# Kernel optimization log

Hardware: AMD Instinct MI355X
Metric: run time of the kernel (lower is better)

Reference implementation:

```python
import jax, jax.numpy as jnp
import numpy as np
import math

PS = 65          # patch_size
NB_ANG = 8       # num_ang_bins
NB_SP = 4        # num_spatial_bins
CLIP = 0.2
EPS = 1e-10
BIN_KS = 2 * (PS // (NB_SP + 1))   # 26
BIN_STRIDE = PS // NB_SP           # 16
BIN_PAD = BIN_KS // 4              # 6


def _gaussian_kernel2d(ks, sigma):
    x = jnp.arange(ks, dtype=jnp.float32) - ks // 2
    if ks % 2 == 0:
        x = x + 0.5
    g = jnp.exp(-(x * x) / (2.0 * sigma * sigma))
    g = g / g.sum()
    return jnp.outer(g, g)  # [ps, ps]


def _sift_pooling_kernel(ks):
    ks2 = ks / 2.0
    xc2 = ks2 - jnp.abs(jnp.arange(ks, dtype=jnp.float32) + 0.5 - ks2)
    return jnp.outer(xc2, xc2) / (ks2 * ks2)  # [26, 26] triangular bilinear kernel


def _l2n(x):
    # torch F.normalize(p=2, dim=-1, eps=1e-12)
    return x / jnp.maximum(jnp.linalg.norm(x, axis=-1, keepdims=True), 1e-12)


def setup_inputs() -> dict:
    key = jax.random.key(0)
    image_batch = jax.random.uniform(key, (16, 3, 520, 520), dtype=jnp.float32)
    return {"image_batch": image_batch}


def reference(image_batch):
    B, C, H, W = image_batch.shape
    nH, nW = H // PS, W // PS
    # torch unfold(2,ps,ps).unfold(3,ps,ps).reshape(-1, c, ps, ps)
    # (row-major reshape replicated exactly, including its channel/patch mixing)
    p = image_batch.reshape(B, C, nH, PS, nW, PS).transpose(0, 1, 2, 4, 3, 5)
    x = p.reshape(-1, C, PS, PS)  # [N, C, ps, ps]; (N,C) treated as independent patches
    N = x.shape[0]

    # kornia spatial_gradient(mode='diff', normalized=True): replicate pad, central diff / 2
    xp = jnp.pad(x, ((0, 0), (0, 0), (1, 1), (1, 1)), mode='edge')
    gx = (xp[:, :, 1:-1, 2:] - xp[:, :, 1:-1, :-2]) * 0.5
    gy = (xp[:, :, 2:, 1:-1] - xp[:, :, :-2, 1:-1]) * 0.5

    mag = jnp.sqrt(gx * gx + gy * gy + EPS)
    ori = jnp.arctan2(gy, gx + EPS) + 2.0 * jnp.pi
    gk = _gaussian_kernel2d(PS, PS / math.sqrt(2.0))
    mag = mag * gk  # Gaussian spatial weighting

    # soft orientation binning
    o_big = (NB_ANG / (2.0 * jnp.pi)) * ori
    bo0f = jnp.floor(o_big)
    wo1 = o_big - bo0f
    bo0 = (bo0f % NB_ANG).astype(jnp.int32)
    bo1 = (bo0 + 1) % NB_ANG
    # [N, C, ps, ps, 8] soft histogram field
    contrib = (jax.nn.one_hot(bo0, NB_ANG, dtype=x.dtype) * ((1.0 - wo1) * mag)[..., None]
               + jax.nn.one_hot(bo1, NB_ANG, dtype=x.dtype) * (wo1 * mag)[..., None])

    # spatial pooling: conv 26x26, stride 16, zero-pad 6 -> 4x4 per angle bin
    contrib = jnp.moveaxis(contrib, -1, 2).reshape(N * C * NB_ANG, 1, PS, PS)
    pk = _sift_pooling_kernel(BIN_KS)[None, None]  # [1,1,26,26]
    pooled = jax.lax.conv_general_dilated(
        contrib, pk,
        window_strides=(BIN_STRIDE, BIN_STRIDE),
        padding=((BIN_PAD, BIN_PAD), (BIN_PAD, BIN_PAD)),
        dimension_numbers=('NCHW', 'OIHW', 'NCHW'))  # [N*C*8, 1, 4, 4]

    desc = pooled.reshape(N, C, NB_ANG * NB_SP * NB_SP)  # [N, C, 128]
    desc = _l2n(desc)
    desc = jnp.clip(desc, 0.0, CLIP)
    desc = _l2n(desc)
    return desc  # [B*nH*nW, C, 128] (root_sift=False)
```

## Files before the change

kernel.cpp:

```cpp
#include <hip/hip_runtime.h>
#include <math.h>

#define PSTR 33

constexpr double cfabs_(double x) { return x < 0 ? -x : x; }
constexpr double cexp_neg(double x) {
    double t = 1.0, s = 1.0;
    for (int i = 1; i < 20; ++i) { t *= (-x) / i; s += t; }
    return s;
}
constexpr double graw(int i) {
    double d = (double)(i - 32);
    return cexp_neg(d * d / 4225.0);
}
constexpr double gsum_() { double s = 0; for (int i = 0; i < 65; ++i) s += graw(i); return s; }
constexpr double GSUM_V = gsum_();
constexpr float gnv(int i) { return (float)(graw(i) / GSUM_V); }

struct WTab { float a[65]; };
constexpr WTab mkw(int sy) {
    WTab w{};
    for (int i = 0; i < 65; ++i) {
        double t = 13.0 - cfabs_((double)i - 16.0 * sy - 6.5);
        w.a[i] = (float)((graw(i) / GSUM_V) * t / 13.0);
    }
    return w;
}
constexpr WTab WGTBL[4] = { mkw(0), mkw(1), mkw(2), mkw(3) };
#define WGTG(SY, RR) (WGTBL[SY].a[RR])
constexpr float G64F = gnv(64);

#define G4_(n) gnv(n), gnv(n+1), gnv(n+2), gnv(n+3)
__device__ __constant__ float d_gtab[65] = {
    G4_(0), G4_(4), G4_(8), G4_(12), G4_(16), G4_(20), G4_(24), G4_(28),
    G4_(32), G4_(36), G4_(40), G4_(44), G4_(48), G4_(52), G4_(56), G4_(60),
    gnv(64)
};

__device__ __forceinline__ float fast_atan2f(float y, float x) {
    float ax = fabsf(x), ay = fabsf(y);
    float mx = fmaxf(ax, ay);
    float mn = fminf(ax, ay);
    float a = mn * __builtin_amdgcn_rcpf(fmaxf(mx, 1e-30f));
    float s = a * a;
    float r = fmaf(s, fmaf(s, fmaf(s, fmaf(s, fmaf(s, -0.0117212f, 0.05265332f),
                    -0.11643287f), 0.19354346f), -0.33262347f), 0.99997726f) * a;
    r = (ay > ax) ? (1.57079637f - r) : r;
    r = (x < 0.0f) ? (3.14159274f - r) : r;
    return copysignf(r, y);
}

template<int CTRL>
__device__ __forceinline__ float upd_dpp(float old, float src) {
    return __uint_as_float((unsigned)__builtin_amdgcn_update_dpp(
        (int)__float_as_uint(old), (int)__float_as_uint(src), CTRL, 0xF, 0xF, false));
}

__device__ __forceinline__ float rdlane_lit(float x, int l) {
    return __uint_as_float((unsigned)__builtin_amdgcn_readlane((int)__float_as_uint(x), l));
}

__device__ __forceinline__ float wave_sum64(float v) {
    v += upd_dpp<0xB1>(v, v);
    v += upd_dpp<0x4E>(v, v);
    v += upd_dpp<0x141>(v, v);
    v += upd_dpp<0x140>(v, v);
    float a = rdlane_lit(v, 0)  + rdlane_lit(v, 16);
    float b = rdlane_lit(v, 32) + rdlane_lit(v, 48);
    return a + b;
}

#define FMA8(P, W)                                                        \
    P##0 = fmaf(s0, (W), P##0); P##1 = fmaf(s1, (W), P##1);               \
    P##2 = fmaf(s2, (W), P##2); P##3 = fmaf(s3, (W), P##3);               \
    P##4 = fmaf(s4, (W), P##4); P##5 = fmaf(s5, (W), P##5);               \
    P##6 = fmaf(s6, (W), P##6); P##7 = fmaf(s7, (W), P##7);

#define RDLC(RR) __uint_as_float((unsigned)__builtin_amdgcn_readlane((int)__float_as_uint(C64), (RR)))

#define PIX(ARR, I, RR, ACCUM)                                            \
    {                                                                     \
        float c64r = ((RR) < 64) ? RDLC((RR) & 63) : c64top;              \
        float xc = ARR[I];                                                \
        float xl = upd_dpp<0x138>(xc, xc);                                \
        float xr = upd_dpp<0x130>(c64r, xc);                              \
        float dx = xr - xl;                                               \
        float dy = ARR[(I) + 1] - ARR[(I) - 1];                           \
        float ax_ = fabsf(dx), ay_ = fabsf(dy);                           \
        float mx = fmaxf(fmaxf(ax_, ay_), 1e-30f);                        \
        float mn = fminf(ax_, ay_);                                       \
        float t = mn * __builtin_amdgcn_rcpf(mx);                         \
        float ts = t * t;                                                 \
        float f = fmaf(ts, fmaf(ts, fmaf(ts, fmaf(ts, fmaf(ts,           \
                  -0.01492344f, 0.06703556f), -0.14824473f), 0.24642112f),\
                  -0.42350443f), 1.27321063f) * t;                        \
        float magw = sqrtf(fmaf(dx, dx, fmaf(dy, dy, 4e-10f))) * GCl;     \
        bool sdb = ay_ > ax_;                                             \
        bool sxb = dx < 0.0f;                                             \
        bool syb = dy < 0.0f;                                             \
        bool midb = sxb != syb;                                           \
        bool parb = sdb != midb;                                          \
        float wo1 = parb ? (1.0f - f) : f;                                \
        float q1 = wo1 * magw;                                            \
        float q0 = magw - q1;                                             \
        bool h0 = !syb && !midb && !parb;                                 \
        bool h1 = !syb && !midb &&  parb;                                 \
        bool h2 = !syb &&  midb && !parb;                                 \
        bool h3 = !syb &&  midb &&  parb;                                 \
        bool h4 =  syb && !midb && !parb;                                 \
        bool h5 =  syb && !midb &&  parb;                                 \
        bool h6 =  syb &&  midb && !parb;                                 \
        bool h7 =  syb &&  midb &&  parb;                                 \
        float s0 = h0 ? q0 : (h7 ? q1 : 0.0f);                            \
        float s1 = h1 ? q0 : (h0 ? q1 : 0.0f);                            \
        float s2 = h2 ? q0 : (h1 ? q1 : 0.0f);                            \
        float s3 = h3 ? q0 : (h2 ? q1 : 0.0f);                            \
        float s4 = h4 ? q0 : (h3 ? q1 : 0.0f);                            \
        float s5 = h5 ? q0 : (h4 ? q1 : 0.0f);                            \
        float s6 = h6 ? q0 : (h5 ? q1 : 0.0f);                            \
        float s7 = h7 ? q0 : (h6 ? q1 : 0.0f);                            \
        ACCUM                                                             \
    }

#define LOAD_RA(BASE)                                                     \
    _Pragma("unroll")                                                     \
    for (int i = 0; i < 18; ++i) {                                        \
        int rr = (BASE) + i; rr = (rr < 0) ? 0 : ((rr > 64) ? 64 : rr);   \
        RA[i] = src[rr * 520 + lane];                                     \
    }
#define LOAD_RB(BASE)                                                     \
    _Pragma("unroll")                                                     \
    for (int i = 0; i < 19; ++i) {                                        \
        int rr = (BASE) + i; rr = (rr < 0) ? 0 : ((rr > 64) ? 64 : rr);   \
        RB[i] = src[rr * 520 + lane];                                     \
    }
#define PIN_RA  _Pragma("unroll") for (int i = 0; i < 18; ++i) asm volatile("" : "+v"(RA[i]));
#define PIN_RB  _Pragma("unroll") for (int i = 0; i < 19; ++i) asm volatile("" : "+v"(RB[i]));

__global__ __launch_bounds__(64)
__attribute__((amdgpu_waves_per_eu(2, 3)))
void sift_kernel(const float* __restrict__ in, float* __restrict__ out) {
    __shared__ float part[65 * PSTR];
    __shared__ float c64buf[67];

    const int lane = threadIdx.x;
    const int m  = blockIdx.x;
    const int bc = m >> 6;
    const int ij = m & 63;
    const float* src = in + (size_t)bc * (520 * 520) + (ij >> 3) * (65 * 520) + (ij & 7) * 65;

    {
        int rr = lane - 1; rr = (rr < 0) ? 0 : rr;
        c64buf[lane] = src[rr * 520 + 64];
        if (lane < 3) {
            int r2 = 63 + lane; r2 = (r2 > 64) ? 64 : r2;
            c64buf[64 + lane] = src[r2 * 520 + 64];
        }
        if (lane < 32) part[64 * PSTR + lane] = 0.0f;
    }
    float C64    = src[lane * 520 + 64];
    float c64top = src[64 * 520 + 64];
    float xl63   = src[lane * 520 + 63];
    float xl63b  = src[64 * 520 + 63];

    float RA[18], RB[19];
    LOAD_RA(-1)
    LOAD_RB(15)

    const float gl  = d_gtab[lane];
    const float g64 = G64F;
    const float GCl = 0.5f * gl;

    const int cb = lane * PSTR;

    float A0=0,A1=0,A2=0,A3=0,A4=0,A5=0,A6=0,A7=0;
    float B0=0,B1=0,B2=0,B3=0,B4=0,B5=0,B6=0,B7=0;
    float C0=0,C1=0,C2=0,C3=0,C4=0,C5=0,C6=0,C7=0;
    float F0=0,F1=0,F2=0,F3=0,F4=0,F5=0,F6=0,F7=0;

    PIN_RA
    #pragma unroll
    for (int r = 0; r < 10; ++r)   PIX(RA, r + 1, r, FMA8(A, WGTG(0, r)))
    #pragma unroll
    for (int r = 10; r < 16; ++r)  PIX(RA, r + 1, r, FMA8(A, WGTG(0, r)) FMA8(B, WGTG(1, r)))

    LOAD_RA(31)
    PIN_RB
    #pragma unroll
    for (int r = 16; r < 20; ++r)  PIX(RB, r - 15, r, FMA8(A, WGTG(0, r)) FMA8(B, WGTG(1, r)))
    #pragma unroll
    for (int r = 20; r < 26; ++r)  PIX(RB, r - 15, r, FMA8(B, WGTG(1, r)))
    #pragma unroll
    for (int r = 26; r < 32; ++r)  PIX(RB, r - 15, r, FMA8(B, WGTG(1, r)) FMA8(C, WGTG(2, r)))
    part[cb + 0] = A0; part[cb + 1] = A1; part[cb + 2] = A2; part[cb + 3] = A3;
    part[cb + 4] = A4; part[cb + 5] = A5; part[cb + 6] = A6; part[cb + 7] = A7;

    LOAD_RB(47)
    PIN_RA
    #pragma unroll
    for (int r = 32; r < 36; ++r)  PIX(RA, r - 31, r, FMA8(B, WGTG(1, r)) FMA8(C, WGTG(2, r)))
    #pragma unroll
    for (int r = 36; r < 42; ++r)  PIX(RA, r - 31, r, FMA8(C, WGTG(2, r)))
    #pragma unroll
    for (int r = 42; r < 48; ++r)  PIX(RA, r - 31, r, FMA8(C, WGTG(2, r)) FMA8(F, WGTG(3, r)))
    part[cb + 8] = B0; part[cb + 9] = B1; part[cb +10] = B2; part[cb +11] = B3;
    part[cb +12] = B4; part[cb +13] = B5; part[cb +14] = B6; part[cb +15] = B7;

    PIN_RB
    #pragma unroll
    for (int r = 48; r < 52; ++r)  PIX(RB, r - 47, r, FMA8(C, WGTG(2, r)) FMA8(F, WGTG(3, r)))
    #pragma unroll
    for (int r = 52; r < 65; ++r)  PIX(RB, r - 47, r, FMA8(F, WGTG(3, r)))
    part[cb +16] = C0; part[cb +17] = C1; part[cb +18] = C2; part[cb +19] = C3;
    part[cb +20] = C4; part[cb +21] = C5; part[cb +22] = C6; part[cb +23] = C7;
    part[cb +24] = F0; part[cb +25] = F1; part[cb +26] = F2; part[cb +27] = F3;
    part[cb +28] = F4; part[cb +29] = F5; part[cb +30] = F6; part[cb +31] = F7;

    {
        int r = lane;
        float xu  = c64buf[r];
        float xcc = c64buf[r + 1];
        float xd  = c64buf[r + 2];
        float dx = xcc - xl63;
        float dy = xd - xu;
        float magw = sqrtf(fmaf(dx, dx, fmaf(dy, dy, 4e-10f))) * (gl * (0.5f * g64));
        float ang = fast_atan2f(dy, dx + 2e-10f);
        float o   = fmaf(ang, 1.27323954f, 8.0f);
        int bi = (int)o;
        float wo1 = o - (float)bi;
        int b0 = bi & 7;
        int b1 = (bi + 1) & 7;
        float q1 = wo1 * magw;
        float q0 = magw - q1;
        float* eb = &part[64 * PSTR];
        int syA = (r + 6) >> 4; if (syA > 3) syA = 3;
        float uA = (float)(r - 16 * syA + 6);
        float wA = (13.0f - fabsf(uA - 12.5f)) * (1.0f / 13.0f);
        atomicAdd(eb + syA * 8 + b0, q0 * wA);
        atomicAdd(eb + syA * 8 + b1, q1 * wA);
        int syB = syA - 1;
        if (syB >= 0) {
            float uB = (float)(r - 16 * syB + 6);
            float wB = (13.0f - fabsf(uB - 12.5f)) * (1.0f / 13.0f);
            if (wB > 0.0f) {
                atomicAdd(eb + syB * 8 + b0, q0 * wB);
                atomicAdd(eb + syB * 8 + b1, q1 * wB);
            }
        }
        if (lane == 0) {
            float xu2  = c64buf[64];
            float xc2  = c64buf[65];
            float xd2  = c64buf[66];
            float dx2 = xc2 - xl63b;
            float dy2 = xd2 - xu2;
            float mg = sqrtf(fmaf(dx2, dx2, fmaf(dy2, dy2, 4e-10f))) * (g64 * (0.5f * g64));
            float an = fast_atan2f(dy2, dx2 + 2e-10f);
            float o2 = fmaf(an, 1.27323954f, 8.0f);
            int bi2 = (int)o2;
            float w1 = o2 - (float)bi2;
            int c0 = bi2 & 7;
            int c1 = (bi2 + 1) & 7;
            float p1 = w1 * mg;
            float p0 = mg - p1;
            const float w64 = 3.5f * (1.0f / 13.0f);
            atomicAdd(eb + 3 * 8 + c0, p0 * w64);
            atomicAdd(eb + 3 * 8 + c1, p1 * w64);
        }
    }

    {
        float v0, v1;
        #pragma unroll
        for (int h = 0; h < 2; ++h) {
            int o  = lane + h * 64;
            int a  = o >> 4;
            int sy = (o >> 2) & 3;
            int sx = o & 3;
            float s = 0.0f;
            #pragma unroll 2
            for (int k = 0; k < 26; ++k) {
                int c = sx * 16 - 6 + k;
                if ((unsigned)c <= 64u) {
                    float wc = (13.0f - fabsf((float)k - 12.5f)) * (1.0f / 13.0f);
                    s = fmaf(wc, part[c * PSTR + sy * 8 + a], s);
                }
            }
            if (h == 0) v0 = s; else v1 = s;
        }
        float ss = wave_sum64(v0 * v0 + v1 * v1);
        float sc = 1.0f / fmaxf(sqrtf(ss), 1e-12f);
        v0 = fminf(fmaxf(v0 * sc, 0.0f), 0.2f);
        v1 = fminf(fmaxf(v1 * sc, 0.0f), 0.2f);
        ss = wave_sum64(v0 * v0 + v1 * v1);
        sc = 1.0f / fmaxf(sqrtf(ss), 1e-12f);
        out[(size_t)m * 128 + lane]      = v0 * sc;
        out[(size_t)m * 128 + lane + 64] = v1 * sc;
    }
}

extern "C" void kernel_launch(void* const* d_in, const int* in_sizes, int n_in,
                              void* d_out, int out_size, void* d_ws, size_t ws_size,
                              hipStream_t stream) {
    const float* in = (const float*)d_in[0];
    float* out = (float*)d_out;
    sift_kernel<<<3072, 64, 0, stream>>>(in, out);
}
```

Baseline: 40.04 us.

## Split patch rows across four waves with LDS atomic accumulation

Each block grows from one wave to four. Each wave processes a 16-row band of the 65x65 patch instead of one wave sweeping all rows. Partial column histograms are merged into shared memory with LDS atomicAdd, and the edge column and bottom row are handled by the bands. This aims to cut per-block serial latency and expose more parallelism per patch, at the cost of zeroing shared memory, extra barriers, and atomic contention.

New measurement: 115.2 us. 188% more time.

```diff
diff --git a/kernel.cpp b/kernel.cpp
--- a/kernel.cpp
+++ b/kernel.cpp
@@ -122,153 +122,169 @@
         ACCUM                                                             \
     }
 
-#define LOAD_RA(BASE)                                                     \
-    _Pragma("unroll")                                                     \
-    for (int i = 0; i < 18; ++i) {                                        \
-        int rr = (BASE) + i; rr = (rr < 0) ? 0 : ((rr > 64) ? 64 : rr);   \
-        RA[i] = src[rr * 520 + lane];                                     \
-    }
-#define LOAD_RB(BASE)                                                     \
-    _Pragma("unroll")                                                     \
-    for (int i = 0; i < 19; ++i) {                                        \
-        int rr = (BASE) + i; rr = (rr < 0) ? 0 : ((rr > 64) ? 64 : rr);   \
-        RB[i] = src[rr * 520 + lane];                                     \
-    }
-#define PIN_RA  _Pragma("unroll") for (int i = 0; i < 18; ++i) asm volatile("" : "+v"(RA[i]));
-#define PIN_RB  _Pragma("unroll") for (int i = 0; i < 19; ++i) asm volatile("" : "+v"(RB[i]));
-
-__global__ __launch_bounds__(64)
+#define AFLUSH8(P, BASE)                                                  \
+    atomicAdd(&part[(BASE) + 0], P##0); atomicAdd(&part[(BASE) + 1], P##1); \
+    atomicAdd(&part[(BASE) + 2], P##2); atomicAdd(&part[(BASE) + 3], P##3); \
+    atomicAdd(&part[(BASE) + 4], P##4); atomicAdd(&part[(BASE) + 5], P##5); \
+    atomicAdd(&part[(BASE) + 6], P##6); atomicAdd(&part[(BASE) + 7], P##7);
+
+__global__ __launch_bounds__(256)
 __attribute__((amdgpu_waves_per_eu(2, 3)))
 void sift_kernel(const float* __restrict__ in, float* __restrict__ out) {
     __shared__ float part[65 * PSTR];
     __shared__ float c64buf[67];
 
-    const int lane = threadIdx.x;
+    const int tid  = threadIdx.x;
+    const int lane = tid & 63;
+    const int wid  = tid >> 6;
     const int m  = blockIdx.x;
     const int bc = m >> 6;
     const int ij = m & 63;
     const float* src = in + (size_t)bc * (520 * 520) + (ij >> 3) * (65 * 520) + (ij & 7) * 65;
 
-    {
-        int rr = lane - 1; rr = (rr < 0) ? 0 : rr;
-        c64buf[lane] = src[rr * 520 + 64];
-        if (lane < 3) {
-            int r2 = 63 + lane; r2 = (r2 > 64) ? 64 : r2;
-            c64buf[64 + lane] = src[r2 * 520 + 64];
-        }
-        if (lane < 32) part[64 * PSTR + lane] = 0.0f;
+    for (int k = tid; k < 65 * PSTR; k += 256) part[k] = 0.0f;
+    if (tid < 67) {
+        int rr = tid - 1; rr = (rr < 0) ? 0 : ((rr > 64) ? 64 : rr);
+        c64buf[tid] = src[rr * 520 + 64];
+    }
+
+    const int r0 = wid * 16;
+    float RA[18];
+    #pragma unroll
+    for (int i = 0; i < 18; ++i) {
+        int rr = r0 - 1 + i;
+        rr = (rr < 0) ? 0 : ((rr > 64) ? 64 : rr);
+        RA[i] = src[rr * 520 + lane];
     }
     float C64    = src[lane * 520 + 64];
     float c64top = src[64 * 520 + 64];
-    float xl63   = src[lane * 520 + 63];
-    float xl63b  = src[64 * 520 + 63];
-
-    float RA[18], RB[19];
-    LOAD_RA(-1)
-    LOAD_RB(15)
-
-    const float gl  = d_gtab[lane];
-    const float g64 = G64F;
-    const float GCl = 0.5f * gl;
-
-    const int cb = lane * PSTR;
+
+    const float GCl = 0.5f * d_gtab[lane];
+
+    #pragma unroll
+    for (int i = 0; i < 18; ++i) asm volatile("" : "+v"(RA[i]));
+
+    __syncthreads();
 
     float A0=0,A1=0,A2=0,A3=0,A4=0,A5=0,A6=0,A7=0;
     float B0=0,B1=0,B2=0,B3=0,B4=0,B5=0,B6=0,B7=0;
     float C0=0,C1=0,C2=0,C3=0,C4=0,C5=0,C6=0,C7=0;
-    float F0=0,F1=0,F2=0,F3=0,F4=0,F5=0,F6=0,F7=0;
-
-    PIN_RA
-    #pragma unroll
-    for (int r = 0; r < 10; ++r)   PIX(RA, r + 1, r, FMA8(A, WGTG(0, r)))
-    #pragma unroll
-    for (int r = 10; r < 16; ++r)  PIX(RA, r + 1, r, FMA8(A, WGTG(0, r)) FMA8(B, WGTG(1, r)))
-
-    LOAD_RA(31)
-    PIN_RB
-    #pragma unroll
-    for (int r = 16; r < 20; ++r)  PIX(RB, r - 15, r, FMA8(A, WGTG(0, r)) FMA8(B, WGTG(1, r)))
-    #pragma unroll
-    for (int r = 20; r < 26; ++r)  PIX(RB, r - 15, r, FMA8(B, WGTG(1, r)))
-    #pragma unroll
-    for (int r = 26; r < 32; ++r)  PIX(RB, r - 15, r, FMA8(B, WGTG(1, r)) FMA8(C, WGTG(2, r)))
-    part[cb + 0] = A0; part[cb + 1] = A1; part[cb + 2] = A2; part[cb + 3] = A3;
-    part[cb + 4] = A4; part[cb + 5] = A5; part[cb + 6] = A6; part[cb + 7] = A7;
-
-    LOAD_RB(47)
-    PIN_RA
-    #pragma unroll
-    for (int r = 32; r < 36; ++r)  PIX(RA, r - 31, r, FMA8(B, WGTG(1, r)) FMA8(C, WGTG(2, r)))
-    #pragma unroll
-    for (int r = 36; r < 42; ++r)  PIX(RA, r - 31, r, FMA8(C, WGTG(2, r)))
-    #pragma unroll
-    for (int r = 42; r < 48; ++r)  PIX(RA, r - 31, r, FMA8(C, WGTG(2, r)) FMA8(F, WGTG(3, r)))
-    part[cb + 8] = B0; part[cb + 9] = B1; part[cb +10] = B2; part[cb +11] = B3;
-    part[cb +12] = B4; part[cb +13] = B5; part[cb +14] = B6; part[cb +15] = B7;
-
-    PIN_RB
-    #pragma unroll
-    for (int r = 48; r < 52; ++r)  PIX(RB, r - 47, r, FMA8(C, WGTG(2, r)) FMA8(F, WGTG(3, r)))
-    #pragma unroll
-    for (int r = 52; r < 65; ++r)  PIX(RB, r - 47, r, FMA8(F, WGTG(3, r)))
-    part[cb +16] = C0; part[cb +17] = C1; part[cb +18] = C2; part[cb +19] = C3;
-    part[cb +20] = C4; part[cb +21] = C5; part[cb +22] = C6; part[cb +23] = C7;
-    part[cb +24] = F0; part[cb +25] = F1; part[cb +26] = F2; part[cb +27] = F3;
-    part[cb +28] = F4; part[cb +29] = F5; part[cb +30] = F6; part[cb +31] = F7;
+
+    if (wid == 0) {
+        #pragma unroll
+        for (int k = 0; k <= 9; ++k)   PIX(RA, k + 1, k, FMA8(B, WGTG(0, k)))
+        #pragma unroll
+        for (int k = 10; k <= 15; ++k) PIX(RA, k + 1, k, FMA8(B, WGTG(0, k)) FMA8(C, WGTG(1, k)))
+    } else if (wid == 1) {
+        #pragma unroll
+        for (int k = 0; k <= 3; ++k)   PIX(RA, k + 1, 16 + k, FMA8(A, WGTG(0, 16 + k)) FMA8(B, WGTG(1, 16 + k)))
+        #pragma unroll
+        for (int k = 4; k <= 9; ++k)   PIX(RA, k + 1, 16 + k, FMA8(B, WGTG(1, 16 + k)))
+        #pragma unroll
+        for (int k = 10; k <= 15; ++k) PIX(RA, k + 1, 16 + k, FMA8(B, WGTG(1, 16 + k)) FMA8(C, WGTG(2, 16 + k)))
+    } else if (wid == 2) {
+        #pragma unroll
+        for (int k = 0; k <= 3; ++k)   PIX(RA, k + 1, 32 + k, FMA8(A, WGTG(1, 32 + k)) FMA8(B, WGTG(2, 32 + k)))
+        #pragma unroll
+        for (int k = 4; k <= 9; ++k)   PIX(RA, k + 1, 32 + k, FMA8(B, WGTG(2, 32 + k)))
+        #pragma unroll
+        for (int k = 10; k <= 15; ++k) PIX(RA, k + 1, 32 + k, FMA8(B, WGTG(2, 32 + k)) FMA8(C, WGTG(3, 32 + k)))
+    } else {
+        #pragma unroll
+        for (int k = 0; k <= 3; ++k)   PIX(RA, k + 1, 48 + k, FMA8(A, WGTG(2, 48 + k)) FMA8(B, WGTG(3, 48 + k)))
+        #pragma unroll
+        for (int k = 4; k <= 15; ++k)  PIX(RA, k + 1, 48 + k, FMA8(B, WGTG(3, 48 + k)))
+        {
+            float c64r = c64top;
+            float xc = RA[17];
+            float xl = upd_dpp<0x138>(xc, xc);
+            float xr = upd_dpp<0x130>(c64r, xc);
+            float dx = xr - xl;
+            float dy = RA[17] - RA[16];
+            float ax_ = fabsf(dx), ay_ = fabsf(dy);
+            float mx = fmaxf(fmaxf(ax_, ay_), 1e-30f);
+            float mn = fminf(ax_, ay_);
+            float t = mn * __builtin_amdgcn_rcpf(mx);
+            float ts = t * t;
+            float f = fmaf(ts, fmaf(ts, fmaf(ts, fmaf(ts, fmaf(ts,
+                      -0.01492344f, 0.06703556f), -0.14824473f), 0.24642112f),
+                      -0.42350443f), 1.27321063f) * t;
+            float magw = sqrtf(fmaf(dx, dx, fmaf(dy, dy, 4e-10f))) * GCl;
+            bool sdb = ay_ > ax_;
+            bool sxb = dx < 0.0f;
+            bool syb = dy < 0.0f;
+            bool midb = sxb != syb;
+            bool parb = sdb != midb;
+            float wo1 = parb ? (1.0f - f) : f;
+            float q1 = wo1 * magw;
+            float q0 = magw - q1;
+            bool h0 = !syb && !midb && !parb;
+            bool h1 = !syb && !midb &&  parb;
+            bool h2 = !syb &&  midb && !parb;
+            bool h3 = !syb &&  midb &&  parb;
+            bool h4 =  syb && !midb && !parb;
+            bool h5 =  syb && !midb &&  parb;
+            bool h6 =  syb &&  midb && !parb;
+            bool h7 =  syb &&  midb &&  parb;
+            float s0 = h0 ? q0 : (h7 ? q1 : 0.0f);
+            float s1 = h1 ? q0 : (h0 ? q1 : 0.0f);
+            float s2 = h2 ? q0 : (h1 ? q1 : 0.0f);
+            float s3 = h3 ? q0 : (h2 ? q1 : 0.0f);
+            float s4 = h4 ? q0 : (h3 ? q1 : 0.0f);
+            float s5 = h5 ? q0 : (h4 ? q1 : 0.0f);
+            float s6 = h6 ? q0 : (h5 ? q1 : 0.0f);
+            float s7 = h7 ? q0 : (h6 ? q1 : 0.0f);
+            FMA8(B, WGTG(3, 64))
+        }
+    }
 
     {
-        int r = lane;
-        float xu  = c64buf[r];
-        float xcc = c64buf[r + 1];
-        float xd  = c64buf[r + 2];
-        float dx = xcc - xl63;
-        float dy = xd - xu;
-        float magw = sqrtf(fmaf(dx, dx, fmaf(dy, dy, 4e-10f))) * (gl * (0.5f * g64));
-        float ang = fast_atan2f(dy, dx + 2e-10f);
-        float o   = fmaf(ang, 1.27323954f, 8.0f);
-        int bi = (int)o;
-        float wo1 = o - (float)bi;
-        int b0 = bi & 7;
-        int b1 = (bi + 1) & 7;
-        float q1 = wo1 * magw;
-        float q0 = magw - q1;
-        float* eb = &part[64 * PSTR];
-        int syA = (r + 6) >> 4; if (syA > 3) syA = 3;
-        float uA = (float)(r - 16 * syA + 6);
-        float wA = (13.0f - fabsf(uA - 12.5f)) * (1.0f / 13.0f);
-        atomicAdd(eb + syA * 8 + b0, q0 * wA);
-        atomicAdd(eb + syA * 8 + b1, q1 * wA);
-        int syB = syA - 1;
-        if (syB >= 0) {
-            float uB = (float)(r - 16 * syB + 6);
-            float wB = (13.0f - fabsf(uB - 12.5f)) * (1.0f / 13.0f);
-            if (wB > 0.0f) {
-                atomicAdd(eb + syB * 8 + b0, q0 * wB);
-                atomicAdd(eb + syB * 8 + b1, q1 * wB);
+        const int cb = lane * PSTR;
+        if (wid > 0) { AFLUSH8(A, cb + (wid - 1) * 8) }
+        AFLUSH8(B, cb + wid * 8)
+        if (wid < 3) { AFLUSH8(C, cb + (wid + 1) * 8) }
+    }
+
+    {
+        const int nr = (wid == 3) ? 17 : 16;
+        if (lane < nr) {
+            int r = r0 + lane;
+            float gnr  = d_gtab[r];
+            float xl63 = src[r * 520 + 63];
+            float xu   = c64buf[r];
+            float xcc  = c64buf[r + 1];
+            float xd   = c64buf[r + 2];
+            float dx = xcc - xl63;
+            float dy = xd - xu;
+            float magw = sqrtf(fmaf(dx, dx, fmaf(dy, dy, 4e-10f))) * (gnr * (0.5f * G64F));
+            float ang = fast_atan2f(dy, dx + 2e-10f);
+            float o   = fmaf(ang, 1.27323954f, 8.0f);
+            int bi = (int)o;
+            float wo1 = o - (float)bi;
+            int b0 = bi & 7;
+            int b1 = (bi + 1) & 7;
+            float q1 = wo1 * magw;
+            float q0 = magw - q1;
+            float* eb = &part[64 * PSTR];
+            int syA = (r + 6) >> 4; if (syA > 3) syA = 3;
+            float uA = (float)(r - 16 * syA + 6);
+            float wA = (13.0f - fabsf(uA - 12.5f)) * (1.0f / 13.0f);
+            atomicAdd(eb + syA * 8 + b0, q0 * wA);
+            atomicAdd(eb + syA * 8 + b1, q1 * wA);
+            int syB = syA - 1;
+            if (syB >= 0) {
+                float uB = (float)(r - 16 * syB + 6);
+                float wB = (13.0f - fabsf(uB - 12.5f)) * (1.0f / 13.0f);
+                if (wB > 0.0f) {
+                    atomicAdd(eb + syB * 8 + b0, q0 * wB);
+                    atomicAdd(eb + syB * 8 + b1, q1 * wB);
+                }
             }
         }
-        if (lane == 0) {
-            float xu2  = c64buf[64];
-            float xc2  = c64buf[65];
-            float xd2  = c64buf[66];
-            float dx2 = xc2 - xl63b;
-            float dy2 = xd2 - xu2;
-            float mg = sqrtf(fmaf(dx2, dx2, fmaf(dy2, dy2, 4e-10f))) * (g64 * (0.5f * g64));
-            float an = fast_atan2f(dy2, dx2 + 2e-10f);
-            float o2 = fmaf(an, 1.27323954f, 8.0f);
-            int bi2 = (int)o2;
-            float w1 = o2 - (float)bi2;
-            int c0 = bi2 & 7;
-            int c1 = (bi2 + 1) & 7;
-            float p1 = w1 * mg;
-            float p0 = mg - p1;
-            const float w64 = 3.5f * (1.0f / 13.0f);
-            atomicAdd(eb + 3 * 8 + c0, p0 * w64);
-            atomicAdd(eb + 3 * 8 + c1, p1 * w64);
-        }
-    }
-
-    {
+    }
+    __syncthreads();
+
+    if (wid == 0) {
         float v0, v1;
         #pragma unroll
         for (int h = 0; h < 2; ++h) {
@@ -303,5 +319,5 @@
                               hipStream_t stream) {
     const float* in = (const float*)d_in[0];
     float* out = (float*)d_out;
-    sift_kernel<<<3072, 64, 0, stream>>>(in, out);
-}
+    sift_kernel<<<3072, 256, 0, stream>>>(in, out);
+}
```
